# Kernel optimization log

Measured on AMD Instinct MI355X. Metric: run time of the kernel, lower is better.

## Reference

```python
import jax, jax.numpy as jnp
import numpy as np

N_NODES = 100000
N_EDGES = 3200000
M = 24
HID = 32
OUT = 16


def neighbor_mean(feat, row, col, num_nodes):
    # sum features of source nodes into destination nodes, divide by in-degree
    sums = jax.ops.segment_sum(feat[row], col, num_segments=num_nodes)  # (N, F)
    deg = jax.ops.segment_sum(jnp.ones_like(col, dtype=feat.dtype), col, num_segments=num_nodes)
    return sums / jnp.clip(deg, 1.0)[:, None]


def sage_conv(x, row, col, num_nodes, w_l, b_l, w_r):
    # PyG SAGEConv(aggr='mean'): lin_l(mean_aggr) + lin_r(x); lin_r has no bias
    aggr = neighbor_mean(x, row, col, num_nodes)
    return aggr @ w_l.T + b_l + x @ w_r.T


def setup_inputs() -> dict:
    key = jax.random.key(0)
    ks = jax.random.split(key, 10)
    x_bin = jax.random.randint(ks[0], (N_NODES, M), 0, 2).astype(jnp.float32)
    edge_index = jax.random.randint(ks[1], (2, N_EDGES), 0, N_NODES).astype(jnp.int64)
    s = 0.1
    return {
        "x_bin": x_bin,
        "edge_index": edge_index,
        "w1l": s * jax.random.normal(ks[2], (HID, M), jnp.float32),
        "b1": s * jax.random.normal(ks[3], (HID,), jnp.float32),
        "w1r": s * jax.random.normal(ks[4], (HID, M), jnp.float32),
        "w2l": s * jax.random.normal(ks[5], (OUT, HID), jnp.float32),
        "b2": s * jax.random.normal(ks[6], (OUT,), jnp.float32),
        "w2r": s * jax.random.normal(ks[7], (OUT, HID), jnp.float32),
        "head_w": s * jax.random.normal(ks[8], (1, 3 * M + OUT), jnp.float32),
        "head_b": s * jax.random.normal(ks[9], (1,), jnp.float32),
    }


def reference(x_bin, edge_index, w1l, b1, w1r, w2l, b2, w2r, head_w, head_b):
    num_nodes = x_bin.shape[0]
    row, col = edge_index[0], edge_index[1]
    # explicit branch: [self markers | neighbor fraction | self * neighbor fraction]
    frac1 = neighbor_mean(x_bin, row, col, num_nodes)
    feats = jnp.concatenate([x_bin, frac1, x_bin * frac1], axis=1)  # (N, 3M)
    # GNN branch: SmallSAGE (dropout is identity at inference)
    h = jax.nn.relu(sage_conv(x_bin, row, col, num_nodes, w1l, b1, w1r))
    emb = jax.nn.relu(sage_conv(h, row, col, num_nodes, w2l, b2, w2r))  # (N, OUT)
    z = jnp.concatenate([feats, emb], axis=1)  # (N, 3M+OUT)
    yhat = (z @ head_w.T + head_b)[:, 0]  # (N,)
    return yhat, z
```

## Files before the change

### kernel.cpp

```cpp
#include <hip/hip_runtime.h>
#include <hip/hip_bf16.h>

#define MF 24
#define HIDF 32
#define OUTF 16
#define ZDIM 88
#define NPB 8
#define NPB2 32
#define SW1 28
#define SW2 36

#define NB 512
#define EB 4096
#define CAP 8192

union bf16x8 {
    float4 v;
    __hip_bfloat16 h[8];
};
union bf16x2u {
    unsigned int u;
    __hip_bfloat16 h[2];
};

__device__ __forceinline__ float ldw(const void* p, size_t i, bool bf16) {
    return bf16 ? __bfloat162float(((const __hip_bfloat16*)p)[i])
                : ((const float*)p)[i];
}

__device__ __forceinline__ bool detect_bf(const unsigned int* __restrict__ xw) {
    unsigned int w = xw[threadIdx.x & 63];
    return __ballot((w & 0xFFFFu) == 0x3F80u) != 0ull;
}
__device__ __forceinline__ bool detect_i64(const unsigned int* __restrict__ ew) {
    unsigned int w = ew[2 * (threadIdx.x & 63) + 1];
    return __popcll(__ballot(w == 0u)) >= 32;
}

__device__ __forceinline__ int bkt_of(int c, unsigned long long Wm) {
    return (int)(((unsigned long long)(unsigned)c * Wm) >> 32);
}

__device__ __forceinline__ float bf_lo(unsigned u) { return __uint_as_float(u << 16); }
__device__ __forceinline__ float bf_hi(unsigned u) { return __uint_as_float(u & 0xFFFF0000u); }

#define HIST_EDGE(c_)                                                   \
    if ((unsigned)(c_) < (unsigned)N) atomicAdd(&hist[bkt_of(c_, Wm)], 1);

__global__ __launch_bounds__(256) void k_histA(
    const void* __restrict__ x, unsigned int* __restrict__ xpack,
    const int* __restrict__ ei, int* __restrict__ counts,
    int nE, int N, unsigned long long Wm) {
    const bool bf16 = detect_bf((const unsigned int*)x);
    const bool i64 = detect_i64((const unsigned int*)ei);

    for (int n = blockIdx.x * 256 + threadIdx.x; n < N; n += gridDim.x * 256) {
        unsigned int m = 0;
        if (bf16) {
            const float4* xr = reinterpret_cast<const float4*>(
                (const __hip_bfloat16*)x + (size_t)n * MF);
            bf16x8 u;
#pragma unroll
            for (int q = 0; q < 3; ++q) {
                u.v = xr[q];
#pragma unroll
                for (int i = 0; i < 8; ++i)
                    if (__bfloat162float(u.h[i]) != 0.f) m |= 1u << (q * 8 + i);
            }
        } else {
            const float* xr = (const float*)x + (size_t)n * MF;
#pragma unroll
            for (int k = 0; k < MF; ++k)
                if (xr[k] != 0.f) m |= 1u << k;
        }
        xpack[n] = m;
    }

    __shared__ int hist[NB];
    for (int i = threadIdx.x; i < NB; i += 256) hist[i] = 0;
    __syncthreads();
    size_t base = (size_t)blockIdx.x * EB;
    int m = nE - (int)base;
    if (m > EB) m = EB;
    if (!(nE & 1)) {
        int nPair = m >> 1;
        if (i64) {
            const int4* cp = (const int4*)ei + (((size_t)nE + base) >> 1);
            for (int j = threadIdx.x; j < nPair; j += 256) {
                int4 c4 = cp[j];
                HIST_EDGE(c4.x);
                HIST_EDGE(c4.z);
            }
        } else {
            const int2* cp = (const int2*)ei + (((size_t)nE + base) >> 1);
            for (int j = threadIdx.x; j < nPair; j += 256) {
                int2 c2 = cp[j];
                HIST_EDGE(c2.x);
                HIST_EDGE(c2.y);
            }
        }
        for (int i = (nPair << 1) + threadIdx.x; i < m; i += 256) {
            size_t e = base + i;
            int c = i64 ? ei[2 * ((size_t)nE + e)] : ei[(size_t)nE + e];
            HIST_EDGE(c);
        }
    } else {
        for (int i = threadIdx.x; i < m; i += 256) {
            size_t e = base + i;
            int c = i64 ? ei[2 * ((size_t)nE + e)] : ei[(size_t)nE + e];
            HIST_EDGE(c);
        }
    }
    __syncthreads();
    for (int i = threadIdx.x; i < NB; i += 256)
        counts[(size_t)blockIdx.x * NB + i] = hist[i];
}

__global__ __launch_bounds__(1024) void k_colscan(int* __restrict__ counts,
                                                  int* __restrict__ colSum, int nBlk) {
    __shared__ int s[1024];
    int b = blockIdx.x, t = threadIdx.x;
    int v = (t < nBlk) ? counts[(size_t)t * NB + b] : 0;
    s[t] = v;
    __syncthreads();
    for (int off = 1; off < 1024; off <<= 1) {
        int y = (t >= off) ? s[t - off] : 0;
        __syncthreads();
        s[t] += y;
        __syncthreads();
    }
    if (t < nBlk) counts[(size_t)t * NB + b] = s[t] - v;
    if (t == 1023) colSum[b] = s[1023];
}

__global__ __launch_bounds__(1024) void k_bstart(const int* __restrict__ colSum,
                                                 int* __restrict__ bucketStart) {
    __shared__ int s[1024];
    int t = threadIdx.x;
    int v = (t < NB) ? colSum[t] : 0;
    s[t] = v;
    __syncthreads();
    for (int off = 1; off < 1024; off <<= 1) {
        int y = (t >= off) ? s[t - off] : 0;
        __syncthreads();
        s[t] += y;
        __syncthreads();
    }
    if (t < NB) bucketStart[t] = s[t] - v;
    if (t == NB - 1) bucketStart[NB] = s[t];
}

#define SCAT_EDGE(r_, c_)                                               \
    if ((unsigned)(c_) < (unsigned)N) {                                 \
        int b_ = bkt_of(c_, Wm);                                        \
        int ld_ = (c_) - b_ * W;                                        \
        unsigned rr_ = ((unsigned)(r_) < (unsigned)N) ? (unsigned)(r_) : 0u; \
        int pos_ = ldsStart[b_] + atomicAdd(&lcnt[b_], 1);              \
        rec[pos_] = rr_ | ((unsigned)ld_ << 20);                        \
        bkt[pos_] = (unsigned short)b_;                                 \
    }

__global__ __launch_bounds__(256) void k_scatB(
    const int* __restrict__ ei, const int* __restrict__ counts,
    const int* __restrict__ colSum, const int* __restrict__ bucketStart,
    unsigned int* __restrict__ part, int nE, int N, int W,
    unsigned long long Wm, int nBlk) {
    const bool i64 = detect_i64((const unsigned int*)ei);
    __shared__ unsigned int rec[EB];
    __shared__ unsigned short bkt[EB];
    __shared__ int ldsStart[NB + 1];
    __shared__ int lcnt[NB];
    __shared__ int base2[NB];
    __shared__ int s256[256];
    const int t = threadIdx.x, blk = blockIdx.x;

    for (int b = t; b < NB; b += 256) {
        int pre = counts[(size_t)blk * NB + b];
        int nxt = (blk + 1 < nBlk) ? counts[(size_t)(blk + 1) * NB + b] : colSum[b];
        ldsStart[b] = nxt - pre;
        lcnt[b] = 0;
        base2[b] = bucketStart[b] + pre;
    }
    __syncthreads();

    int v0 = ldsStart[2 * t], v1 = ldsStart[2 * t + 1];
    int pairSum = v0 + v1;
    s256[t] = pairSum;
    __syncthreads();
    for (int off = 1; off < 256; off <<= 1) {
        int y = (t >= off) ? s256[t - off] : 0;
        __syncthreads();
        s256[t] += y;
        __syncthreads();
    }
    int base = s256[t] - pairSum;
    ldsStart[2 * t] = base;
    ldsStart[2 * t + 1] = base + v0;
    if (t == 255) ldsStart[NB] = base + pairSum;
    __syncthreads();
    for (int b = t; b < NB; b += 256) base2[b] -= ldsStart[b];
    __syncthreads();

    size_t eb = (size_t)blk * EB;
    int m = nE - (int)eb;
    if (m > EB) m = EB;
    if (!(nE & 1)) {
        int nPair = m >> 1;
        if (i64) {
            const int4* rp = (const int4*)ei + (eb >> 1);
            const int4* cp = (const int4*)ei + (((size_t)nE + eb) >> 1);
            for (int j = t; j < nPair; j += 256) {
                int4 r4 = rp[j];
                int4 c4 = cp[j];
                SCAT_EDGE(r4.x, c4.x);
                SCAT_EDGE(r4.z, c4.z);
            }
        } else {
            const int2* rp = (const int2*)ei + (eb >> 1);
            const int2* cp = (const int2*)ei + (((size_t)nE + eb) >> 1);
            for (int j = t; j < nPair; j += 256) {
                int2 r2 = rp[j];
                int2 c2 = cp[j];
                SCAT_EDGE(r2.x, c2.x);
                SCAT_EDGE(r2.y, c2.y);
            }
        }
        for (int i = (nPair << 1) + t; i < m; i += 256) {
            size_t e = eb + i;
            int r = i64 ? ei[2 * e] : ei[e];
            int c = i64 ? ei[2 * ((size_t)nE + e)] : ei[(size_t)nE + e];
            SCAT_EDGE(r, c);
        }
    } else {
        for (int i = t; i < m; i += 256) {
            size_t e = eb + i;
            int r = i64 ? ei[2 * e] : ei[e];
            int c = i64 ? ei[2 * ((size_t)nE + e)] : ei[(size_t)nE + e];
            SCAT_EDGE(r, c);
        }
    }
    __syncthreads();

    int total = ldsStart[NB];
    for (int i = t; i < total; i += 256) {
        int b = bkt[i];
        part[base2[b] + i] = rec[i];
    }
}

__global__ __launch_bounds__(256) void k_csrC(const int* __restrict__ bucketStart,
                                              unsigned int* __restrict__ part,
                                              int* __restrict__ degi,
                                              int* __restrict__ rowstart,
                                              const unsigned int* __restrict__ xpack,
                                              unsigned int* __restrict__ cnt3,
                                              int N, int W) {
    __shared__ unsigned int stage[CAP];
    __shared__ unsigned int c3[256 * 6];
    __shared__ int hist[256];
    __shared__ int sc[256];
    __shared__ int cur[256];
    int b = blockIdx.x, t = threadIdx.x;
    int start = bucketStart[b];
    int bs = bucketStart[b + 1] - start;
    int node = b * W + t;

    hist[t] = 0;
#pragma unroll
    for (int j = 0; j < 6; ++j) c3[t * 6 + j] = 0;
    __syncthreads();

    if (bs > CAP) {
        if (t < W && node < N) {
            degi[node] = 0; rowstart[node] = start;
#pragma unroll
            for (int j = 0; j < 6; ++j) cnt3[(size_t)node * 6 + j] = 0;
        }
        return;
    }

    for (int i = t; i < bs; i += 256) {
        unsigned int v = part[start + i];
        stage[i] = v;
        int ld = v >> 20;
        atomicAdd(&hist[ld], 1);
        unsigned int xp = xpack[v & 0xFFFFFu];
        int b3 = ld * 6;
#pragma unroll
        for (int j = 0; j < 6; ++j) {
            unsigned int nib = (xp >> (4 * j)) & 0xFu;
            atomicAdd(&c3[b3 + j], (nib * 0x00204081u) & 0x01010101u);
        }
    }
    __syncthreads();

    int v = hist[t];
    sc[t] = v;
    __syncthreads();
    for (int off = 1; off < 256; off <<= 1) {
        int y = (t >= off) ? sc[t - off] : 0;
        __syncthreads();
        sc[t] += y;
        __syncthreads();
    }
    int excl = sc[t] - v;
    if (t < W && node < N) {
        degi[node] = v;
        rowstart[node] = start + excl;
#pragma unroll
        for (int j = 0; j < 6; ++j) cnt3[(size_t)node * 6 + j] = c3[t * 6 + j];
    }
    cur[t] = excl;
    __syncthreads();

    for (int i = t; i < bs; i += 256) {
        unsigned int v2 = stage[i];
        int pos = atomicAdd(&cur[v2 >> 20], 1);
        part[start + pos] = v2 & 0xFFFFFu;
    }
}

__global__ __launch_bounds__(256) void k_layer1(
    const void* __restrict__ x, const unsigned int* __restrict__ xpack,
    const int* __restrict__ degi, const unsigned int* __restrict__ cnt3,
    void* __restrict__ out,
    const void* __restrict__ w1l, const void* __restrict__ b1,
    const void* __restrict__ w1r, const void* __restrict__ w2l,
    const void* __restrict__ b2, const void* __restrict__ w2r,
    const void* __restrict__ head_w,
    __hip_bfloat16* __restrict__ hl, __hip_bfloat16* __restrict__ st,
    float* __restrict__ ypart, int N) {
    const bool bf16 = detect_bf((const unsigned int*)x);
    __shared__ float swl[HIDF * SW1];
    __shared__ float swr[HIDF * SW1];
    __shared__ float sb[HIDF];
    __shared__ float s2l[OUTF * SW2];
    __shared__ float s2r[OUTF * SW2];
    __shared__ float sb2[OUTF];
    __shared__ float shw[3 * MF];
    __shared__ float fs[NPB][MF];
    __shared__ float hs[NPB][HIDF];
    const int t = threadIdx.x;

    if (bf16) {
        const uint4* al = (const uint4*)w1l;
        const uint4* ar = (const uint4*)w1r;
        if (t < 96) {
            uint4 vl = al[t], vr = ar[t];
            int i0 = t * 8;
            int j = i0 / MF, k = i0 - j * MF;
            float4 fl0 = make_float4(bf_lo(vl.x), bf_hi(vl.x), bf_lo(vl.y), bf_hi(vl.y));
            float4 fl1 = make_float4(bf_lo(vl.z), bf_hi(vl.z), bf_lo(vl.w), bf_hi(vl.w));
            float4 fr0 = make_float4(bf_lo(vr.x), bf_hi(vr.x), bf_lo(vr.y), bf_hi(vr.y));
            float4 fr1 = make_float4(bf_lo(vr.z), bf_hi(vr.z), bf_lo(vr.w), bf_hi(vr.w));
            float4* dl = (float4*)(swl + j * SW1 + k);
            float4* dr = (float4*)(swr + j * SW1 + k);
            dl[0] = fl0; dl[1] = fl1;
            dr[0] = fr0; dr[1] = fr1;
        }
        const uint4* bl = (const uint4*)w2l;
        const uint4* br = (const uint4*)w2r;
        if (t >= 128 && t < 192) {
            int c = t - 128;
            uint4 vl = bl[c], vr = br[c];
            int i0 = c * 8;
            int o = i0 >> 5, j = i0 & 31;
            float4 fl0 = make_float4(bf_lo(vl.x), bf_hi(vl.x), bf_lo(vl.y), bf_hi(vl.y));
            float4 fl1 = make_float4(bf_lo(vl.z), bf_hi(vl.z), bf_lo(vl.w), bf_hi(vl.w));
            float4 fr0 = make_float4(bf_lo(vr.x), bf_hi(vr.x), bf_lo(vr.y), bf_hi(vr.y));
            float4 fr1 = make_float4(bf_lo(vr.z), bf_hi(vr.z), bf_lo(vr.w), bf_hi(vr.w));
            float4* dl = (float4*)(s2l + o * SW2 + j);
            float4* dr = (float4*)(s2r + o * SW2 + j);
            dl[0] = fl0; dl[1] = fl1;
            dr[0] = fr0; dr[1] = fr1;
        }
    } else {
        const float4* al = (const float4*)w1l;
        const float4* ar = (const float4*)w1r;
        if (t < 192) {
            float4 vl = al[t], vr = ar[t];
            int i0 = t * 4;
            int j = i0 / MF, k = i0 - j * MF;
            *(float4*)(swl + j * SW1 + k) = vl;
            *(float4*)(swr + j * SW1 + k) = vr;
        }
        const float4* bl = (const float4*)w2l;
        const float4* br = (const float4*)w2r;
        int c = t - 128;
        if (c >= 0 && c < 128) {
            float4 vl = bl[c], vr = br[c];
            int i0 = c * 4;
            int o = i0 >> 5, j = i0 & 31;
            *(float4*)(s2l + o * SW2 + j) = vl;
            *(float4*)(s2r + o * SW2 + j) = vr;
        }
    }
    if (t < HIDF) sb[t] = ldw(b1, t, bf16);
    if (t >= 64 && t < 64 + OUTF) sb2[t - 64] = ldw(b2, t - 64, bf16);
    if (t >= 96 && t < 96 + 3 * MF) shw[t - 96] = ldw(head_w, t - 96, bf16);
    __syncthreads();

    const int lane = threadIdx.x & 31;
    const int wg = threadIdx.x >> 5;
    int node = blockIdx.x * NPB + wg;
    bool valid = node < N;

    int dg = 0;
    unsigned int xpn = 0;
    unsigned int cw = 0;
    if (valid) {
        dg = degi[node];
        xpn = xpack[node];
        if (lane < MF) cw = cnt3[(size_t)node * 6 + (lane >> 2)];
    }
    int cnt = (cw >> ((lane & 3) * 8)) & 0xFF;

    float inv = 1.f / fmaxf((float)dg, 1.f);
    float fv = (float)cnt * inv;
    float xv = (float)((xpn >> lane) & 1);

    float pc = 0.f;
    if (valid && lane < MF) {
        if (bf16) {
            __hip_bfloat16* z = (__hip_bfloat16*)out + N + (size_t)node * ZDIM;
            z[lane] = __float2bfloat16(xv);
            z[MF + lane] = __float2bfloat16(fv);
            z[2 * MF + lane] = __float2bfloat16(xv * fv);
        } else {
            float* z = (float*)out + N + (size_t)node * ZDIM;
            z[lane] = xv;
            z[MF + lane] = fv;
            z[2 * MF + lane] = xv * fv;
        }
        pc = xv * shw[lane] + fv * shw[MF + lane] + xv * fv * shw[2 * MF + lane];
    }

    if (lane < MF) fs[wg][lane] = fv;

    float fvk[MF];
    {
        const float4* fp = (const float4*)fs[wg];
#pragma unroll
        for (int q = 0; q < 6; ++q) {
            float4 f4 = fp[q];
            fvk[q * 4 + 0] = f4.x; fvk[q * 4 + 1] = f4.y;
            fvk[q * 4 + 2] = f4.z; fvk[q * 4 + 3] = f4.w;
        }
    }
    float wlv[MF], wrv[MF];
    {
        const float4* wl4 = (const float4*)(swl + lane * SW1);
        const float4* wr4 = (const float4*)(swr + lane * SW1);
#pragma unroll
        for (int q = 0; q < 6; ++q) {
            float4 a = wl4[q], b = wr4[q];
            wlv[q * 4 + 0] = a.x; wlv[q * 4 + 1] = a.y;
            wlv[q * 4 + 2] = a.z; wlv[q * 4 + 3] = a.w;
            wrv[q * 4 + 0] = b.x; wrv[q * 4 + 1] = b.y;
            wrv[q * 4 + 2] = b.z; wrv[q * 4 + 3] = b.w;
        }
    }
    float acc = sb[lane];
#pragma unroll
    for (int k = 0; k < MF; ++k) {
        acc = fmaf(fvk[k], wlv[k], acc);
        acc += ((xpn >> k) & 1u) ? wrv[k] : 0.f;
    }
    hs[wg][lane] = fmaxf(acc, 0.f);

#pragma unroll
    for (int off = 16; off > 0; off >>= 1) pc += __shfl_down(pc, off, 32);

    int o = lane & 15;
    int half = lane >> 4;
    const float4* wrow4 = (const float4*)((half ? s2r : s2l) + o * SW2);
    const float4* hp4 = (const float4*)hs[wg];
    float d = 0.f;
#pragma unroll
    for (int q = 0; q < 8; ++q) {
        float4 hq = hp4[q], wq = wrow4[q];
        d += hq.x * wq.x + hq.y * wq.y + hq.z * wq.z + hq.w * wq.w;
    }
    if (valid) {
        if (half == 0) hl[(size_t)node * OUTF + o] = __float2bfloat16(d);
        else st[(size_t)node * OUTF + o] = __float2bfloat16(d + sb2[o]);
        if (lane == 0) ypart[node] = pc;
    }
}

__global__ __launch_bounds__(256) void k_layer2(
    const void* __restrict__ x, const int* __restrict__ degi,
    const int* __restrict__ rowstart, const unsigned int* __restrict__ srcs,
    const __hip_bfloat16* __restrict__ hl, const __hip_bfloat16* __restrict__ st,
    const float* __restrict__ ypart, void* __restrict__ out,
    const void* __restrict__ head_w, const void* __restrict__ head_b, int N) {
    const bool bf16 = detect_bf((const unsigned int*)x);
    __shared__ float shw2[OUTF];
    __shared__ float shb;
    if (threadIdx.x < OUTF) shw2[threadIdx.x] = ldw(head_w, 3 * MF + threadIdx.x, bf16);
    if (threadIdx.x == 0) shb = ldw(head_b, 0, bf16);
    __syncthreads();

    int lane = threadIdx.x & 7;
    int g = threadIdx.x >> 3;
    int node = blockIdx.x * NPB2 + g;
    bool valid = node < N;

    int dg = 0, p0 = 0;
    if (valid) {
        dg = degi[node];
        p0 = rowstart[node];
    }
    const unsigned int* hlw = (const unsigned int*)hl;
    float s0 = 0.f, s1 = 0.f;
    int e = 0;
    for (; e + 8 <= dg; e += 8) {
        int i0 = srcs[p0 + e],     i1 = srcs[p0 + e + 1];
        int i2 = srcs[p0 + e + 2], i3 = srcs[p0 + e + 3];
        int i4 = srcs[p0 + e + 4], i5 = srcs[p0 + e + 5];
        int i6 = srcs[p0 + e + 6], i7 = srcs[p0 + e + 7];
        bf16x2u u0, u1, u2, u3, u4, u5, u6, u7;
        u0.u = hlw[(size_t)i0 * 8 + lane];
        u1.u = hlw[(size_t)i1 * 8 + lane];
        u2.u = hlw[(size_t)i2 * 8 + lane];
        u3.u = hlw[(size_t)i3 * 8 + lane];
        u4.u = hlw[(size_t)i4 * 8 + lane];
        u5.u = hlw[(size_t)i5 * 8 + lane];
        u6.u = hlw[(size_t)i6 * 8 + lane];
        u7.u = hlw[(size_t)i7 * 8 + lane];
        s0 += (__bfloat162float(u0.h[0]) + __bfloat162float(u1.h[0])) +
              (__bfloat162float(u2.h[0]) + __bfloat162float(u3.h[0])) +
              (__bfloat162float(u4.h[0]) + __bfloat162float(u5.h[0])) +
              (__bfloat162float(u6.h[0]) + __bfloat162float(u7.h[0]));
        s1 += (__bfloat162float(u0.h[1]) + __bfloat162float(u1.h[1])) +
              (__bfloat162float(u2.h[1]) + __bfloat162float(u3.h[1])) +
              (__bfloat162float(u4.h[1]) + __bfloat162float(u5.h[1])) +
              (__bfloat162float(u6.h[1]) + __bfloat162float(u7.h[1]));
    }
    for (; e + 4 <= dg; e += 4) {
        int a = srcs[p0 + e], b = srcs[p0 + e + 1];
        int c = srcs[p0 + e + 2], d = srcs[p0 + e + 3];
        bf16x2u ua, ub, uc, ud;
        ua.u = hlw[(size_t)a * 8 + lane];
        ub.u = hlw[(size_t)b * 8 + lane];
        uc.u = hlw[(size_t)c * 8 + lane];
        ud.u = hlw[(size_t)d * 8 + lane];
        s0 += (__bfloat162float(ua.h[0]) + __bfloat162float(ub.h[0])) +
              (__bfloat162float(uc.h[0]) + __bfloat162float(ud.h[0]));
        s1 += (__bfloat162float(ua.h[1]) + __bfloat162float(ub.h[1])) +
              (__bfloat162float(uc.h[1]) + __bfloat162float(ud.h[1]));
    }
    for (; e < dg; ++e) {
        bf16x2u ua;
        ua.u = hlw[(size_t)srcs[p0 + e] * 8 + lane];
        s0 += __bfloat162float(ua.h[0]);
        s1 += __bfloat162float(ua.h[1]);
    }

    float emb0 = 0.f, emb1 = 0.f;
    if (valid) {
        float inv = 1.f / fmaxf((float)dg, 1.f);
        bf16x2u us;
        us.u = ((const unsigned int*)st)[(size_t)node * 8 + lane];
        emb0 = fmaxf(s0 * inv + __bfloat162float(us.h[0]), 0.f);
        emb1 = fmaxf(s1 * inv + __bfloat162float(us.h[1]), 0.f);
        if (bf16) {
            bf16x2u up;
            up.h[0] = __float2bfloat16(emb0);
            up.h[1] = __float2bfloat16(emb1);
            unsigned int* zw = (unsigned int*)((__hip_bfloat16*)out + N +
                                               (size_t)node * ZDIM + 3 * MF);
            zw[lane] = up.u;
        } else {
            float2* zw = (float2*)((float*)out + N + (size_t)node * ZDIM + 3 * MF);
            zw[lane] = make_float2(emb0, emb1);
        }
    }
    float part = emb0 * shw2[2 * lane] + emb1 * shw2[2 * lane + 1];
#pragma unroll
    for (int off = 4; off > 0; off >>= 1) part += __shfl_down(part, off, 8);
    if (valid && lane == 0) {
        float y = ypart[node] + part + shb;
        if (bf16) ((__hip_bfloat16*)out)[node] = __float2bfloat16(y);
        else ((float*)out)[node] = y;
    }
}

extern "C" void kernel_launch(void* const* d_in, const int* in_sizes, int n_in,
                              void* d_out, int out_size, void* d_ws, size_t ws_size,
                              hipStream_t stream) {
    const void* x = d_in[0];
    const int* ei = (const int*)d_in[1];
    const void* w1l = d_in[2];
    const void* b1 = d_in[3];
    const void* w1r = d_in[4];
    const void* w2l = d_in[5];
    const void* b2 = d_in[6];
    const void* w2r = d_in[7];
    const void* head_w = d_in[8];
    const void* head_b = d_in[9];

    const int N = in_sizes[0] / MF;
    const int nE = in_sizes[1] / 2;
    const int W = (N + NB - 1) / NB;
    const unsigned long long Wm = (0x100000000ull / (unsigned)W) + 1;
    const int nBlkA = (nE + EB - 1) / EB;

    if (N > NB * 256 || N > 131072 || nBlkA > 1024 ||
        (size_t)nBlkA * NB < (size_t)N || nE < 64) return;

    int* bucketStart = (int*)((char*)d_ws + 256);
    int* colSum = bucketStart + (NB + 1);
    int* degi = colSum + NB;
    int* rowstart = degi + N;
    int* counts = rowstart + N;
    unsigned int* part = (unsigned int*)(counts + (size_t)nBlkA * NB);
    unsigned int* xpack = part + nE;
    __hip_bfloat16* hl = (__hip_bfloat16*)(xpack + N);
    __hip_bfloat16* st = hl + (size_t)N * OUTF;
    unsigned int* cnt3 = (unsigned int*)(st + (size_t)N * OUTF);
    float* ypart = (float*)counts;

    const size_t need = 256 +
        ((size_t)(NB + 1) + NB + 2 * (size_t)N + (size_t)nBlkA * NB +
         (size_t)nE + (size_t)N + 6 * (size_t)N) * 4 + (size_t)N * OUTF * 2 * 2;
    if (ws_size < need) return;

    const int gb1 = (N + NPB - 1) / NPB;
    const int gb2 = (N + NPB2 - 1) / NPB2;
    k_histA<<<nBlkA, 256, 0, stream>>>(x, xpack, ei, counts, nE, N, Wm);
    k_colscan<<<NB, 1024, 0, stream>>>(counts, colSum, nBlkA);
    k_bstart<<<1, 1024, 0, stream>>>(colSum, bucketStart);
    k_scatB<<<nBlkA, 256, 0, stream>>>(ei, counts, colSum, bucketStart,
                                       part, nE, N, W, Wm, nBlkA);
    k_csrC<<<NB, 256, 0, stream>>>(bucketStart, part, degi, rowstart,
                                   xpack, cnt3, N, W);
    k_layer1<<<gb1, 256, 0, stream>>>(x, xpack, degi, cnt3, d_out,
                                      w1l, b1, w1r, w2l, b2, w2r, head_w,
                                      hl, st, ypart, N);
    k_layer2<<<gb2, 256, 0, stream>>>(x, degi, rowstart, part, hl, st, ypart,
                                      d_out, head_w, head_b, N);
}
```

Baseline: 223.9 us.

## Fold bucket-start scan into scatter and CSR kernels, pack LDS counters to 64-bit

Removes the single-block k_bstart launch. Each k_scatB block now recomputes the exclusive scan of colSum itself, and each k_csrC block gets its start offset by reducing colSum over the preceding buckets. The per-node bit-count accumulators in k_csrC are packed into three 64-bit LDS atomics instead of six 32-bit ones, halving the atomic count. The cost is redundant scan and reduction work in every block plus extra barriers, in exchange for one fewer launch and stream serialization point.

```diff
diff --git a/kernel.cpp b/kernel.cpp
--- a/kernel.cpp
+++ b/kernel.cpp
@@ -133,23 +133,6 @@
     if (t == 1023) colSum[b] = s[1023];
 }
 
-__global__ __launch_bounds__(1024) void k_bstart(const int* __restrict__ colSum,
-                                                 int* __restrict__ bucketStart) {
-    __shared__ int s[1024];
-    int t = threadIdx.x;
-    int v = (t < NB) ? colSum[t] : 0;
-    s[t] = v;
-    __syncthreads();
-    for (int off = 1; off < 1024; off <<= 1) {
-        int y = (t >= off) ? s[t - off] : 0;
-        __syncthreads();
-        s[t] += y;
-        __syncthreads();
-    }
-    if (t < NB) bucketStart[t] = s[t] - v;
-    if (t == NB - 1) bucketStart[NB] = s[t];
-}
-
 #define SCAT_EDGE(r_, c_)                                               \
     if ((unsigned)(c_) < (unsigned)N) {                                 \
         int b_ = bkt_of(c_, Wm);                                        \
@@ -162,7 +145,7 @@
 
 __global__ __launch_bounds__(256) void k_scatB(
     const int* __restrict__ ei, const int* __restrict__ counts,
-    const int* __restrict__ colSum, const int* __restrict__ bucketStart,
+    const int* __restrict__ colSum,
     unsigned int* __restrict__ part, int nE, int N, int W,
     unsigned long long Wm, int nBlk) {
     const bool i64 = detect_i64((const unsigned int*)ei);
@@ -174,30 +157,49 @@
     __shared__ int s256[256];
     const int t = threadIdx.x, blk = blockIdx.x;
 
+    {
+        int a0 = colSum[2 * t], a1 = colSum[2 * t + 1];
+        int ps = a0 + a1;
+        s256[t] = ps;
+        __syncthreads();
+        for (int off = 1; off < 256; off <<= 1) {
+            int y = (t >= off) ? s256[t - off] : 0;
+            __syncthreads();
+            s256[t] += y;
+            __syncthreads();
+        }
+        int base = s256[t] - ps;
+        ldsStart[2 * t] = base;
+        ldsStart[2 * t + 1] = base + a0;
+        __syncthreads();
+    }
     for (int b = t; b < NB; b += 256) {
-        int pre = counts[(size_t)blk * NB + b];
-        int nxt = (blk + 1 < nBlk) ? counts[(size_t)(blk + 1) * NB + b] : colSum[b];
-        ldsStart[b] = nxt - pre;
+        base2[b] = ldsStart[b] + counts[(size_t)blk * NB + b];
         lcnt[b] = 0;
-        base2[b] = bucketStart[b] + pre;
-    }
-    __syncthreads();
-
-    int v0 = ldsStart[2 * t], v1 = ldsStart[2 * t + 1];
-    int pairSum = v0 + v1;
-    s256[t] = pairSum;
-    __syncthreads();
-    for (int off = 1; off < 256; off <<= 1) {
-        int y = (t >= off) ? s256[t - off] : 0;
-        __syncthreads();
-        s256[t] += y;
-        __syncthreads();
-    }
-    int base = s256[t] - pairSum;
-    ldsStart[2 * t] = base;
-    ldsStart[2 * t + 1] = base + v0;
-    if (t == 255) ldsStart[NB] = base + pairSum;
-    __syncthreads();
+    }
+    __syncthreads();
+
+    {
+        int p0 = counts[(size_t)blk * NB + 2 * t];
+        int p1 = counts[(size_t)blk * NB + 2 * t + 1];
+        int n0 = (blk + 1 < nBlk) ? counts[(size_t)(blk + 1) * NB + 2 * t] : colSum[2 * t];
+        int n1 = (blk + 1 < nBlk) ? counts[(size_t)(blk + 1) * NB + 2 * t + 1] : colSum[2 * t + 1];
+        int v0 = n0 - p0, v1 = n1 - p1;
+        int ps = v0 + v1;
+        s256[t] = ps;
+        __syncthreads();
+        for (int off = 1; off < 256; off <<= 1) {
+            int y = (t >= off) ? s256[t - off] : 0;
+            __syncthreads();
+            s256[t] += y;
+            __syncthreads();
+        }
+        int base = s256[t] - ps;
+        ldsStart[2 * t] = base;
+        ldsStart[2 * t + 1] = base + v0;
+        if (t == 255) ldsStart[NB] = base + ps;
+        __syncthreads();
+    }
     for (int b = t; b < NB; b += 256) base2[b] -= ldsStart[b];
     __syncthreads();
 
@@ -248,7 +250,7 @@
     }
 }
 
-__global__ __launch_bounds__(256) void k_csrC(const int* __restrict__ bucketStart,
+__global__ __launch_bounds__(256) void k_csrC(const int* __restrict__ colSum,
                                               unsigned int* __restrict__ part,
                                               int* __restrict__ degi,
                                               int* __restrict__ rowstart,
@@ -256,18 +258,26 @@
                                               unsigned int* __restrict__ cnt3,
                                               int N, int W) {
     __shared__ unsigned int stage[CAP];
-    __shared__ unsigned int c3[256 * 6];
+    __shared__ unsigned long long c3[256 * 3];
     __shared__ int hist[256];
     __shared__ int sc[256];
     __shared__ int cur[256];
     int b = blockIdx.x, t = threadIdx.x;
-    int start = bucketStart[b];
-    int bs = bucketStart[b + 1] - start;
+
+    int p = ((t < b) ? colSum[t] : 0) + ((t + 256 < b) ? colSum[t + 256] : 0);
+    sc[t] = p;
+    __syncthreads();
+    for (int off = 128; off > 0; off >>= 1) {
+        if (t < off) sc[t] += sc[t + off];
+        __syncthreads();
+    }
+    int start = sc[0];
+    int bs = colSum[b];
     int node = b * W + t;
 
     hist[t] = 0;
 #pragma unroll
-    for (int j = 0; j < 6; ++j) c3[t * 6 + j] = 0;
+    for (int j = 0; j < 3; ++j) c3[t * 3 + j] = 0ull;
     __syncthreads();
 
     if (bs > CAP) {
@@ -285,11 +295,15 @@
         int ld = v >> 20;
         atomicAdd(&hist[ld], 1);
         unsigned int xp = xpack[v & 0xFFFFFu];
-        int b3 = ld * 6;
-#pragma unroll
-        for (int j = 0; j < 6; ++j) {
-            unsigned int nib = (xp >> (4 * j)) & 0xFu;
-            atomicAdd(&c3[b3 + j], (nib * 0x00204081u) & 0x01010101u);
+        int b3 = ld * 3;
+#pragma unroll
+        for (int j = 0; j < 3; ++j) {
+            unsigned int nlo = (xp >> (8 * j)) & 0xFu;
+            unsigned int nhi = (xp >> (8 * j + 4)) & 0xFu;
+            unsigned long long inc =
+                (unsigned long long)((nlo * 0x00204081u) & 0x01010101u) |
+                ((unsigned long long)((nhi * 0x00204081u) & 0x01010101u) << 32);
+            atomicAdd(&c3[b3 + j], inc);
         }
     }
     __syncthreads();
@@ -307,8 +321,9 @@
     if (t < W && node < N) {
         degi[node] = v;
         rowstart[node] = start + excl;
-#pragma unroll
-        for (int j = 0; j < 6; ++j) cnt3[(size_t)node * 6 + j] = c3[t * 6 + j];
+        const unsigned int* c3w = (const unsigned int*)c3;
+#pragma unroll
+        for (int j = 0; j < 6; ++j) cnt3[(size_t)node * 6 + j] = c3w[t * 6 + j];
     }
     cur[t] = excl;
     __syncthreads();
@@ -609,8 +624,7 @@
     if (N > NB * 256 || N > 131072 || nBlkA > 1024 ||
         (size_t)nBlkA * NB < (size_t)N || nE < 64) return;
 
-    int* bucketStart = (int*)((char*)d_ws + 256);
-    int* colSum = bucketStart + (NB + 1);
+    int* colSum = (int*)((char*)d_ws + 256);
     int* degi = colSum + NB;
     int* rowstart = degi + N;
     int* counts = rowstart + N;
@@ -622,7 +636,7 @@
     float* ypart = (float*)counts;
 
     const size_t need = 256 +
-        ((size_t)(NB + 1) + NB + 2 * (size_t)N + (size_t)nBlkA * NB +
+        ((size_t)NB + 2 * (size_t)N + (size_t)nBlkA * NB +
          (size_t)nE + (size_t)N + 6 * (size_t)N) * 4 + (size_t)N * OUTF * 2 * 2;
     if (ws_size < need) return;
 
@@ -630,10 +644,9 @@
     const int gb2 = (N + NPB2 - 1) / NPB2;
     k_histA<<<nBlkA, 256, 0, stream>>>(x, xpack, ei, counts, nE, N, Wm);
     k_colscan<<<NB, 1024, 0, stream>>>(counts, colSum, nBlkA);
-    k_bstart<<<1, 1024, 0, stream>>>(colSum, bucketStart);
-    k_scatB<<<nBlkA, 256, 0, stream>>>(ei, counts, colSum, bucketStart,
+    k_scatB<<<nBlkA, 256, 0, stream>>>(ei, counts, colSum,
                                        part, nE, N, W, Wm, nBlkA);
-    k_csrC<<<NB, 256, 0, stream>>>(bucketStart, part, degi, rowstart,
+    k_csrC<<<NB, 256, 0, stream>>>(colSum, part, degi, rowstart,
                                    xpack, cnt3, N, W);
     k_layer1<<<gb1, 256, 0, stream>>>(x, xpack, degi, cnt3, d_out,
                                       w1l, b1, w1r, w2l, b2, w2r, head_w,
```

Result: faster. 217.5 us (-2.9%).
